# Kernel tuning notes

Measured on AMD Instinct MI355X. Metric: run time of the kernel, lower is better.

The kernel has to match this reference:

```python
import jax, jax.numpy as jnp
from jax import lax
import numpy as np

B, P, M1, M2, M3 = 128, 168, 2, 2, 2
M = M1 * M2 * M3
HIDC, HIDR, HIDS, CK, SKIP, HW = 50, 50, 5, 6, 24, 24
PT = (P - CK) // SKIP  # int((P-Ck)/skip) = 6
L = P - CK + 1         # 163


def gru(xs, w_ih, w_hh, b_ih, b_hh, hid):
    # xs: [T, N, in]; torch nn.GRU cell semantics, h0 = 0. Returns final h: [N, hid].
    def step(h, x):
        gi = x @ w_ih.T + b_ih
        gh = h @ w_hh.T + b_hh
        ir, iz, inn = jnp.split(gi, 3, axis=-1)
        hr, hz, hn = jnp.split(gh, 3, axis=-1)
        r = jax.nn.sigmoid(ir + hr)
        z = jax.nn.sigmoid(iz + hz)
        n = jnp.tanh(inn + r * hn)
        return (1.0 - z) * n + z * h, None
    h0 = jnp.zeros((xs.shape[1], hid), xs.dtype)
    h, _ = lax.scan(step, h0, xs)
    return h


def setup_inputs() -> dict:
    key = jax.random.key(0)
    ks = jax.random.split(key, 16)
    O = P * HIDC * CK  # 50400 conv output channels
    d = {
        'x': jax.random.normal(ks[0], (B, P, M1, M2, M3), jnp.float32),
        'conv_w': jax.random.normal(ks[1], (O, P, M1, M2, M3), jnp.float32) * 0.02,
        'conv_b': jax.random.normal(ks[2], (O,), jnp.float32) * 0.02,
        'g1_wih': jax.random.normal(ks[3], (3 * HIDR, HIDC), jnp.float32) * 0.1,
        'g1_whh': jax.random.normal(ks[4], (3 * HIDR, HIDR), jnp.float32) * 0.1,
        'g1_bih': jax.random.normal(ks[5], (3 * HIDR,), jnp.float32) * 0.1,
        'g1_bhh': jax.random.normal(ks[6], (3 * HIDR,), jnp.float32) * 0.1,
        'gs_wih': jax.random.normal(ks[7], (3 * HIDS, HIDC), jnp.float32) * 0.1,
        'gs_whh': jax.random.normal(ks[8], (3 * HIDS, HIDS), jnp.float32) * 0.1,
        'gs_bih': jax.random.normal(ks[9], (3 * HIDS,), jnp.float32) * 0.1,
        'gs_bhh': jax.random.normal(ks[10], (3 * HIDS,), jnp.float32) * 0.1,
        'l1_w': jax.random.normal(ks[11], (M, HIDR + SKIP * HIDS), jnp.float32) * 0.1,
        'l1_b': jax.random.normal(ks[12], (M,), jnp.float32) * 0.1,
        'hw_w': jax.random.normal(ks[13], (1, HW), jnp.float32) * 0.1,
        'hw_b': jax.random.normal(ks[14], (1,), jnp.float32) * 0.1,
    }
    return d


def reference(x, conv_w, conv_b, g1_wih, g1_whh, g1_bih, g1_bhh,
              gs_wih, gs_whh, gs_bih, gs_bhh, l1_w, l1_b, hw_w, hw_b):
    # Conv3d with kernel == full spatial extent is a dense matmul over (P*m1*m2*m3).
    xf = x.reshape(B, -1)                       # [B, P*M]
    wf = conv_w.reshape(conv_w.shape[0], -1)    # [O, P*M]
    c = jax.nn.relu(xf @ wf.T + conv_b)         # [B, O]
    c = c.reshape(B, HIDC, CK, P)
    # Diagonal strided sum (the torch triple loop): res1[b,c,t] = sum_k c[b,c,k,k+t]
    res1 = sum(c[:, :, k, k:k + L] for k in range(CK))  # [B, HIDC, L]
    # dropout: eval mode (identity)
    r = gru(jnp.transpose(res1, (2, 0, 1)), g1_wih, g1_whh, g1_bih, g1_bhh, HIDR)  # [B, HIDR]
    # skip GRU
    s = res1[:, :, -PT * SKIP:]                          # [B, HIDC, PT*SKIP]
    s = s.reshape(B, HIDC, PT, SKIP)
    s = jnp.transpose(s, (2, 0, 3, 1)).reshape(PT, B * SKIP, HIDC)
    hs = gru(s, gs_wih, gs_whh, gs_bih, gs_bhh, HIDS)    # [B*SKIP, HIDS]
    hs = hs.reshape(B, SKIP * HIDS)
    r = jnp.concatenate([r, hs], axis=1)                 # [B, HIDR + SKIP*HIDS]
    res = r @ l1_w.T + l1_b                              # [B, M]
    # highway (AR) component over the last HW timesteps
    z = x[:, -HW:].reshape(B, HW, M)                     # [B, HW, M]
    z = jnp.transpose(z, (0, 2, 1)).reshape(-1, HW)      # [B*M, HW]
    z = z @ hw_w.T + hw_b                                # [B*M, 1]
    res = res + z.reshape(B, M)
    res = jax.nn.sigmoid(res)
    return res.reshape(B, M1, M2, M3)
```

## Files before the change

### kernel.cpp

```cpp
#include <hip/hip_runtime.h>
#include <hip/hip_bf16.h>
#include <cstdint>


typedef __attribute__((ext_vector_type(8))) short short8;
typedef __attribute__((ext_vector_type(4))) float f32x4;

__device__ __forceinline__ unsigned short bf16rn(float f) {
    unsigned u = __float_as_uint(f);
    return (unsigned short)((u + 0x7FFFu + ((u >> 16) & 1u)) >> 16);
}
__device__ __forceinline__ unsigned pk2(float a, float b) {
    return ((unsigned)bf16rn(b) << 16) | (unsigned)bf16rn(a);
}
__device__ __forceinline__ uint4 pack8(float4 f0, float4 f1) {
    uint4 u;
    u.x = pk2(f0.x, f0.y); u.y = pk2(f0.z, f0.w);
    u.z = pk2(f1.x, f1.y); u.w = pk2(f1.z, f1.w);
    return u;
}
__device__ __forceinline__ float bf2f(unsigned short u) {
    return __uint_as_float((unsigned)u << 16);
}
__device__ __forceinline__ float sigmf(float x) { return 1.f / (1.f + __expf(-x)); }
__device__ __forceinline__ float tanhf_(float x) { return 1.f - 2.f / (__expf(2.f * x) + 1.f); }

__global__ __launch_bounds__(256, 2)
void k1_conv_gemm(const float* __restrict__ x, const float* __restrict__ w,
                  const float* __restrict__ bias, unsigned short* __restrict__ c) {
    __shared__ uint4 a_lds[8 * 129];
    __shared__ uint4 b_lds[8 * 113];
    const int tid  = threadIdx.x;
    const int n0   = blockIdx.x * 112;
    const int wave = tid >> 6, lane = tid & 63;
    const int quad = lane >> 4, m16 = lane & 15;

    f32x4 acc[2][7];
#pragma unroll
    for (int i = 0; i < 2; ++i)
#pragma unroll
        for (int j = 0; j < 7; ++j) acc[i][j] = (f32x4){0.f, 0.f, 0.f, 0.f};

    float4 pa[4][2];
    float4 pb[4][2];

    auto issue = [&](int kb) {
#pragma unroll
        for (int i = 0; i < 4; ++i) {
            int row = (tid >> 3) + 32 * i;
            const float* gp = x + row * 1344 + kb + (tid & 7) * 8;
            pa[i][0] = *reinterpret_cast<const float4*>(gp);
            pa[i][1] = *reinterpret_cast<const float4*>(gp + 4);
        }
#pragma unroll
        for (int i = 0; i < 4; ++i) {
            int idx = tid + 256 * i;
            if (idx < 896) {
                int row = idx >> 3;
                const float* gp = w + (size_t)(n0 + row) * 1344 + kb + (idx & 7) * 8;
                pb[i][0] = *reinterpret_cast<const float4*>(gp);
                pb[i][1] = *reinterpret_cast<const float4*>(gp + 4);
            }
        }
    };

    issue(0);
    for (int kb = 0; kb < 1344; kb += 64) {
#pragma unroll
        for (int i = 0; i < 4; ++i) {
            int idx = tid + 256 * i;
            int row = idx >> 3, ks = idx & 7;
            a_lds[ks * 129 + row] = pack8(pa[i][0], pa[i][1]);
        }
#pragma unroll
        for (int i = 0; i < 4; ++i) {
            int idx = tid + 256 * i;
            if (idx < 896) {
                int row = idx >> 3, ks = idx & 7;
                b_lds[ks * 113 + row] = pack8(pb[i][0], pb[i][1]);
            }
        }
        __syncthreads();
        if (kb + 64 < 1344) issue(kb + 64);
#pragma unroll
        for (int half = 0; half < 2; ++half) {
            const int kp = half * 4 + quad;
            short8 af[2], bfr[7];
#pragma unroll
            for (int rt = 0; rt < 2; ++rt)
                af[rt] = ((const short8*)a_lds)[kp * 129 + wave * 32 + rt * 16 + m16];
#pragma unroll
            for (int ct = 0; ct < 7; ++ct)
                bfr[ct] = ((const short8*)b_lds)[kp * 113 + ct * 16 + m16];
#pragma unroll
            for (int rt = 0; rt < 2; ++rt)
#pragma unroll
                for (int ct = 0; ct < 7; ++ct)
                    acc[rt][ct] = __builtin_amdgcn_mfma_f32_16x16x32_bf16(
                        af[rt], bfr[ct], acc[rt][ct], 0, 0, 0);
        }
        __syncthreads();
    }
#pragma unroll
    for (int ct = 0; ct < 7; ++ct) {
        int col = n0 + ct * 16 + m16;
        float bv = bias[col];
#pragma unroll
        for (int rt = 0; rt < 2; ++rt) {
#pragma unroll
            for (int r = 0; r < 4; ++r) {
                int grow = wave * 32 + rt * 16 + quad * 4 + r;
                float v = acc[rt][ct][r] + bv;
                v = fmaxf(v, 0.f);
                c[(size_t)grow * 50400 + col] = bf16rn(v);
            }
        }
    }
}

__global__ __launch_bounds__(256)
void k2_diag(const unsigned short* __restrict__ c, float* __restrict__ res1) {
    __shared__ float rloc[50 * 164];
    const int b = blockIdx.x;
    const unsigned short* cb = c + (size_t)b * 50400;
    for (int idx = threadIdx.x; idx < 8150; idx += 256) {
        int hc = idx / 163, t = idx - hc * 163;
        int base = hc * 1008 + t;
        float s = 0.f;
#pragma unroll
        for (int k = 0; k < 6; ++k) s += bf2f(cb[base + 169 * k]);
        rloc[hc * 164 + t] = s;
    }
    __syncthreads();
    for (int idx = threadIdx.x; idx < 8150; idx += 256) {
        int t = idx / 50, hc = idx - t * 50;
        res1[(size_t)(t * 128 + b) * 50 + hc] = rloc[hc * 164 + t];
    }
}

__global__ __launch_bounds__(256)
void k3_gi1(const float* __restrict__ res1, const float* __restrict__ wih,
            const float* __restrict__ bih, float* __restrict__ gi1) {
    __shared__ float wl[150 * 52];
    __shared__ float xl[64 * 52];
    const int row0 = blockIdx.x * 64;
    for (int idx = threadIdx.x; idx < 7500; idx += 256) {
        int r = idx / 50, j = idx - r * 50;
        wl[r * 52 + j] = wih[idx];
    }
    for (int idx = threadIdx.x; idx < 3200; idx += 256) {
        int r = idx / 50, j = idx - r * 50;
        xl[r * 52 + j] = res1[(size_t)row0 * 50 + idx];
    }
    __syncthreads();
    for (int e = threadIdx.x; e < 9600; e += 256) {
        int rr = e / 150, cc = e - rr * 150;
        float4 a0 = {0.f, 0.f, 0.f, 0.f};
        const float* xp = &xl[rr * 52];
        const float* wp = &wl[cc * 52];
#pragma unroll
        for (int j = 0; j < 48; j += 4) {
            float4 xv = *reinterpret_cast<const float4*>(xp + j);
            float4 wv = *reinterpret_cast<const float4*>(wp + j);
            a0.x += xv.x * wv.x; a0.y += xv.y * wv.y;
            a0.z += xv.z * wv.z; a0.w += xv.w * wv.w;
        }
        float acc = bih[cc] + xp[48] * wp[48] + xp[49] * wp[49]
                  + (a0.x + a0.y) + (a0.z + a0.w);
        gi1[(size_t)(row0 + rr) * 150 + cc] = acc;
    }
}

__global__ __launch_bounds__(256)
void k3_gi2(const float* __restrict__ res1, const float* __restrict__ wih,
            const float* __restrict__ bih, float* __restrict__ gi2) {
    __shared__ float wl[15 * 52];
    __shared__ float xl[64 * 52];
    const int row0 = blockIdx.x * 64;
    for (int idx = threadIdx.x; idx < 750; idx += 256) {
        int r = idx / 50, j = idx - r * 50;
        wl[r * 52 + j] = wih[idx];
    }
    for (int idx = threadIdx.x; idx < 3200; idx += 256) {
        int rr = idx / 50, j = idx - rr * 50;
        int r = row0 + rr;
        int pt = r / 3072, bsk = r - pt * 3072;
        int b = bsk / 24, sk = bsk - b * 24;
        int t = 19 + pt * 24 + sk;
        xl[rr * 52 + j] = res1[(size_t)(t * 128 + b) * 50 + j];
    }
    __syncthreads();
    for (int e = threadIdx.x; e < 960; e += 256) {
        int rr = e / 15, cc = e - rr * 15;
        float4 a0 = {0.f, 0.f, 0.f, 0.f};
        const float* xp = &xl[rr * 52];
        const float* wp = &wl[cc * 52];
#pragma unroll
        for (int j = 0; j < 48; j += 4) {
            float4 xv = *reinterpret_cast<const float4*>(xp + j);
            float4 wv = *reinterpret_cast<const float4*>(wp + j);
            a0.x += xv.x * wv.x; a0.y += xv.y * wv.y;
            a0.z += xv.z * wv.z; a0.w += xv.w * wv.w;
        }
        float acc = bih[cc] + xp[48] * wp[48] + xp[49] * wp[49]
                  + (a0.x + a0.y) + (a0.z + a0.w);
        gi2[(size_t)(row0 + rr) * 15 + cc] = acc;
    }
}

__global__ __launch_bounds__(64)
void k4_gru1(const float* __restrict__ gi1, const float* __restrict__ whh,
             const float* __restrict__ bhh, float* __restrict__ r1) {
    __shared__ float wl[7500];
    __shared__ __align__(16) float hl[2][64];
    const int b = blockIdx.x;
    const int l = threadIdx.x;
    for (int idx = l; idx < 7500; idx += 64) wl[idx] = whh[idx];
    hl[0][l] = 0.f;
    hl[1][l] = 0.f;
    __syncthreads();
    const int lc = (l < 50) ? l : 49;
    float wr[50], wz[50], wn[50];
#pragma unroll
    for (int j = 0; j < 50; ++j) {
        wr[j] = wl[lc * 50 + j];
        wz[j] = wl[(50 + lc) * 50 + j];
        wn[j] = wl[(100 + lc) * 50 + j];
    }
    const float bhr = bhh[lc], bhz = bhh[50 + lc], bhn = bhh[100 + lc];
    float hcur = 0.f;
    const float* gp = gi1 + (size_t)b * 150;
    float gir = gp[lc], giz = gp[50 + lc], gin = gp[100 + lc];
    int p = 0;
    for (int t = 0; t < 163; ++t) {
        float ngir = 0.f, ngiz = 0.f, ngin = 0.f;
        if (t < 162) {
            const float* gq = gp + 150 * 128;
            ngir = gq[lc]; ngiz = gq[50 + lc]; ngin = gq[100 + lc];
        }
        const float* hp = hl[p];
        float ar = bhr, az = bhz, an = bhn;
#pragma unroll
        for (int j4 = 0; j4 < 12; ++j4) {
            float4 hv = *reinterpret_cast<const float4*>(hp + 4 * j4);
            ar += wr[4 * j4 + 0] * hv.x + wr[4 * j4 + 1] * hv.y +
                  wr[4 * j4 + 2] * hv.z + wr[4 * j4 + 3] * hv.w;
            az += wz[4 * j4 + 0] * hv.x + wz[4 * j4 + 1] * hv.y +
                  wz[4 * j4 + 2] * hv.z + wz[4 * j4 + 3] * hv.w;
            an += wn[4 * j4 + 0] * hv.x + wn[4 * j4 + 1] * hv.y +
                  wn[4 * j4 + 2] * hv.z + wn[4 * j4 + 3] * hv.w;
        }
        {
            float h48 = hp[48], h49 = hp[49];
            ar += wr[48] * h48 + wr[49] * h49;
            az += wz[48] * h48 + wz[49] * h49;
            an += wn[48] * h48 + wn[49] * h49;
        }
        float rg = sigmf(gir + ar);
        float zg = sigmf(giz + az);
        float ng = tanhf_(gin + rg * an);
        float hn = (1.f - zg) * ng + zg * hcur;
        hl[1 - p][l] = hn;
        __syncthreads();
        p ^= 1;
        hcur = hn;
        gir = ngir; giz = ngiz; gin = ngin;
        gp += 150 * 128;
    }
    if (l < 50) r1[b * 50 + l] = hcur;
}

__global__ __launch_bounds__(256)
void k5_gru2(const float* __restrict__ gi2, const float* __restrict__ whh,
             const float* __restrict__ bhh, float* __restrict__ hs) {
    __shared__ float wl[75];
    __shared__ float bl[15];
    const int tid = threadIdx.x;
    if (tid < 75) wl[tid] = whh[tid];
    if (tid < 15) bl[tid] = bhh[tid];
    __syncthreads();
    const int bsk = blockIdx.x * 256 + tid;
    float h[5] = {0.f, 0.f, 0.f, 0.f, 0.f};
    for (int pt = 0; pt < 6; ++pt) {
        const float* gp = gi2 + (size_t)(pt * 3072 + bsk) * 15;
        float gi[15];
#pragma unroll
        for (int i = 0; i < 15; ++i) gi[i] = gp[i];
        float gh[15];
#pragma unroll
        for (int i = 0; i < 15; ++i) {
            float s = bl[i];
#pragma unroll
            for (int j = 0; j < 5; ++j) s += wl[i * 5 + j] * h[j];
            gh[i] = s;
        }
#pragma unroll
        for (int u = 0; u < 5; ++u) {
            float rg = sigmf(gi[u] + gh[u]);
            float zg = sigmf(gi[5 + u] + gh[5 + u]);
            float ng = tanhf_(gi[10 + u] + rg * gh[10 + u]);
            h[u] = (1.f - zg) * ng + zg * h[u];
        }
    }
#pragma unroll
    for (int u = 0; u < 5; ++u) hs[bsk * 5 + u] = h[u];
}

__global__ __launch_bounds__(256)
void k6_final(const float* __restrict__ r1, const float* __restrict__ hs,
              const float* __restrict__ l1w, const float* __restrict__ l1b,
              const float* __restrict__ x, const float* __restrict__ hww,
              const float* __restrict__ hwb, float* __restrict__ out) {
    const int tid = blockIdx.x * 256 + threadIdx.x;
    if (tid >= 1024) return;
    const int b = tid >> 3, m = tid & 7;
    float acc = l1b[m];
    const float* wrow = l1w + m * 170;
    const float* rb = r1 + b * 50;
#pragma unroll
    for (int j = 0; j < 50; ++j) acc += rb[j] * wrow[j];
    const float* hb = hs + b * 120;
#pragma unroll
    for (int j = 0; j < 120; ++j) acc += hb[j] * wrow[50 + j];
    float z = hwb[0];
    const float* xb = x + b * 1344 + 144 * 8 + m;
#pragma unroll
    for (int wi = 0; wi < 24; ++wi) z += xb[wi * 8] * hww[wi];
    out[tid] = 1.f / (1.f + __expf(-(acc + z)));
}

extern "C" void kernel_launch(void* const* d_in, const int* in_sizes, int n_in,
                              void* d_out, int out_size, void* d_ws, size_t ws_size,
                              hipStream_t stream) {
    const float* x      = (const float*)d_in[0];
    const float* conv_w = (const float*)d_in[1];
    const float* conv_b = (const float*)d_in[2];
    const float* g1_wih = (const float*)d_in[3];
    const float* g1_whh = (const float*)d_in[4];
    const float* g1_bih = (const float*)d_in[5];
    const float* g1_bhh = (const float*)d_in[6];
    const float* gs_wih = (const float*)d_in[7];
    const float* gs_whh = (const float*)d_in[8];
    const float* gs_bih = (const float*)d_in[9];
    const float* gs_bhh = (const float*)d_in[10];
    const float* l1_w   = (const float*)d_in[11];
    const float* l1_b   = (const float*)d_in[12];
    const float* hw_w   = (const float*)d_in[13];
    const float* hw_b   = (const float*)d_in[14];
    float* out = (float*)d_out;

    char* ws = (char*)d_ws;
    unsigned short* c   = (unsigned short*)(ws);
    float* res1         = (float*)(ws + 12902400);
    float* gi1          = (float*)(ws + 17075200);
    float* gi2          = (float*)(ws + 29593600);
    float* r1           = (float*)(ws + 30699520);
    float* hs           = (float*)(ws + 30725120);

    hipLaunchKernelGGL(k1_conv_gemm, dim3(450), dim3(256), 0, stream, x, conv_w, conv_b, c);
    hipLaunchKernelGGL(k2_diag,      dim3(128), dim3(256), 0, stream, c, res1);
    hipLaunchKernelGGL(k3_gi1,       dim3(326), dim3(256), 0, stream, res1, g1_wih, g1_bih, gi1);
    hipLaunchKernelGGL(k3_gi2,       dim3(288), dim3(256), 0, stream, res1, gs_wih, gs_bih, gi2);
    hipLaunchKernelGGL(k4_gru1,      dim3(128), dim3(64),  0, stream, gi1, g1_whh, g1_bhh, r1);
    hipLaunchKernelGGL(k5_gru2,      dim3(12),  dim3(256), 0, stream, gi2, gs_whh, gs_bhh, hs);
    hipLaunchKernelGGL(k6_final,     dim3(4),   dim3(256), 0, stream, r1, hs, l1_w, l1_b, x, hw_w, hw_b, out);
}
```

Baseline: 588.1 us.

## Fuse diagonal sum with GRU input projections into one per-batch kernel

Merges the diagonal strided-sum kernel with both GRU input-gate projection kernels, so each batch block keeps its res1 tile in shared memory and computes gi1 and gi2 directly. This removes the res1 global round trip and two kernel launches. In exchange the gi1 projection runs as a serial 163-step loop per thread over only 128 blocks, which lowers parallelism, and some threads in each block sit idle.

```diff
diff --git a/kernel.cpp b/kernel.cpp
--- a/kernel.cpp
+++ b/kernel.cpp
@@ -119,92 +119,79 @@
 }
 
 __global__ __launch_bounds__(256)
-void k2_diag(const unsigned short* __restrict__ c, float* __restrict__ res1) {
-    __shared__ float rloc[50 * 164];
+void k2f(const unsigned short* __restrict__ c,
+         const float* __restrict__ g1_wih, const float* __restrict__ g1_bih,
+         const float* __restrict__ gs_wih, const float* __restrict__ gs_bih,
+         float* __restrict__ gi1, float* __restrict__ gi2) {
+    __shared__ float xl[163 * 52];
+    __shared__ float wl1[150 * 52];
+    __shared__ float wl2[15 * 52];
+    __shared__ float bl2[15];
     const int b = blockIdx.x;
+    const int tid = threadIdx.x;
     const unsigned short* cb = c + (size_t)b * 50400;
-    for (int idx = threadIdx.x; idx < 8150; idx += 256) {
+
+    for (int i = tid; i < 7500; i += 256) {
+        int r = i / 50, j = i - r * 50;
+        wl1[r * 52 + j] = g1_wih[i];
+    }
+    for (int i = tid; i < 750; i += 256) {
+        int r = i / 50, j = i - r * 50;
+        wl2[r * 52 + j] = gs_wih[i];
+    }
+    if (tid < 15) bl2[tid] = gs_bih[tid];
+    for (int idx = tid; idx < 8150; idx += 256) {
         int hc = idx / 163, t = idx - hc * 163;
         int base = hc * 1008 + t;
         float s = 0.f;
 #pragma unroll
         for (int k = 0; k < 6; ++k) s += bf2f(cb[base + 169 * k]);
-        rloc[hc * 164 + t] = s;
+        xl[t * 52 + hc] = s;
     }
     __syncthreads();
-    for (int idx = threadIdx.x; idx < 8150; idx += 256) {
-        int t = idx / 50, hc = idx - t * 50;
-        res1[(size_t)(t * 128 + b) * 50 + hc] = rloc[hc * 164 + t];
-    }
-}
-
-__global__ __launch_bounds__(256)
-void k3_gi1(const float* __restrict__ res1, const float* __restrict__ wih,
-            const float* __restrict__ bih, float* __restrict__ gi1) {
-    __shared__ float wl[150 * 52];
-    __shared__ float xl[64 * 52];
-    const int row0 = blockIdx.x * 64;
-    for (int idx = threadIdx.x; idx < 7500; idx += 256) {
-        int r = idx / 50, j = idx - r * 50;
-        wl[r * 52 + j] = wih[idx];
-    }
-    for (int idx = threadIdx.x; idx < 3200; idx += 256) {
-        int r = idx / 50, j = idx - r * 50;
-        xl[r * 52 + j] = res1[(size_t)row0 * 50 + idx];
-    }
-    __syncthreads();
-    for (int e = threadIdx.x; e < 9600; e += 256) {
-        int rr = e / 150, cc = e - rr * 150;
-        float4 a0 = {0.f, 0.f, 0.f, 0.f};
-        const float* xp = &xl[rr * 52];
-        const float* wp = &wl[cc * 52];
-#pragma unroll
-        for (int j = 0; j < 48; j += 4) {
-            float4 xv = *reinterpret_cast<const float4*>(xp + j);
-            float4 wv = *reinterpret_cast<const float4*>(wp + j);
-            a0.x += xv.x * wv.x; a0.y += xv.y * wv.y;
-            a0.z += xv.z * wv.z; a0.w += xv.w * wv.w;
-        }
-        float acc = bih[cc] + xp[48] * wp[48] + xp[49] * wp[49]
-                  + (a0.x + a0.y) + (a0.z + a0.w);
-        gi1[(size_t)(row0 + rr) * 150 + cc] = acc;
-    }
-}
-
-__global__ __launch_bounds__(256)
-void k3_gi2(const float* __restrict__ res1, const float* __restrict__ wih,
-            const float* __restrict__ bih, float* __restrict__ gi2) {
-    __shared__ float wl[15 * 52];
-    __shared__ float xl[64 * 52];
-    const int row0 = blockIdx.x * 64;
-    for (int idx = threadIdx.x; idx < 750; idx += 256) {
-        int r = idx / 50, j = idx - r * 50;
-        wl[r * 52 + j] = wih[idx];
-    }
-    for (int idx = threadIdx.x; idx < 3200; idx += 256) {
-        int rr = idx / 50, j = idx - rr * 50;
-        int r = row0 + rr;
-        int pt = r / 3072, bsk = r - pt * 3072;
-        int b = bsk / 24, sk = bsk - b * 24;
-        int t = 19 + pt * 24 + sk;
-        xl[rr * 52 + j] = res1[(size_t)(t * 128 + b) * 50 + j];
-    }
-    __syncthreads();
-    for (int e = threadIdx.x; e < 960; e += 256) {
-        int rr = e / 15, cc = e - rr * 15;
-        float4 a0 = {0.f, 0.f, 0.f, 0.f};
-        const float* xp = &xl[rr * 52];
-        const float* wp = &wl[cc * 52];
-#pragma unroll
-        for (int j = 0; j < 48; j += 4) {
-            float4 xv = *reinterpret_cast<const float4*>(xp + j);
-            float4 wv = *reinterpret_cast<const float4*>(wp + j);
-            a0.x += xv.x * wv.x; a0.y += xv.y * wv.y;
-            a0.z += xv.z * wv.z; a0.w += xv.w * wv.w;
-        }
-        float acc = bih[cc] + xp[48] * wp[48] + xp[49] * wp[49]
-                  + (a0.x + a0.y) + (a0.z + a0.w);
-        gi2[(size_t)(row0 + rr) * 15 + cc] = acc;
+
+    if (tid < 150) {
+        const int cc = tid;
+        float wr[50];
+#pragma unroll
+        for (int j = 0; j < 48; j += 4)
+            *reinterpret_cast<float4*>(&wr[j]) =
+                *reinterpret_cast<const float4*>(&wl1[cc * 52 + j]);
+        wr[48] = wl1[cc * 52 + 48]; wr[49] = wl1[cc * 52 + 49];
+        const float bv = g1_bih[cc];
+        float* gout = gi1 + (size_t)b * 150 + cc;
+        for (int t = 0; t < 163; ++t) {
+            const float* xp = &xl[t * 52];
+            float4 a = {0.f, 0.f, 0.f, 0.f};
+#pragma unroll
+            for (int j = 0; j < 48; j += 4) {
+                float4 xv = *reinterpret_cast<const float4*>(xp + j);
+                a.x += xv.x * wr[j + 0]; a.y += xv.y * wr[j + 1];
+                a.z += xv.z * wr[j + 2]; a.w += xv.w * wr[j + 3];
+            }
+            float acc = bv + xp[48] * wr[48] + xp[49] * wr[49]
+                      + (a.x + a.y) + (a.z + a.w);
+            gout[(size_t)t * 128 * 150] = acc;
+        }
+    } else if (tid >= 192) {
+        for (int e = tid - 192; e < 2160; e += 64) {
+            int rr = e / 15, cc = e - rr * 15;
+            int pt = rr / 24, sk = rr - pt * 24;
+            int t = 19 + pt * 24 + sk;
+            const float* xp = &xl[t * 52];
+            const float* wp = &wl2[cc * 52];
+            float4 a = {0.f, 0.f, 0.f, 0.f};
+#pragma unroll
+            for (int j = 0; j < 48; j += 4) {
+                float4 xv = *reinterpret_cast<const float4*>(xp + j);
+                float4 wv = *reinterpret_cast<const float4*>(wp + j);
+                a.x += xv.x * wv.x; a.y += xv.y * wv.y;
+                a.z += xv.z * wv.z; a.w += xv.w * wv.w;
+            }
+            float acc = bl2[cc] + xp[48] * wp[48] + xp[49] * wp[49]
+                      + (a.x + a.y) + (a.z + a.w);
+            gi2[(size_t)(pt * 3072 + b * 24 + sk) * 15 + cc] = acc;
+        }
     }
 }
 
@@ -351,16 +338,14 @@
 
     char* ws = (char*)d_ws;
     unsigned short* c   = (unsigned short*)(ws);
-    float* res1         = (float*)(ws + 12902400);
-    float* gi1          = (float*)(ws + 17075200);
-    float* gi2          = (float*)(ws + 29593600);
-    float* r1           = (float*)(ws + 30699520);
-    float* hs           = (float*)(ws + 30725120);
+    float* gi1          = (float*)(ws + 12902400);
+    float* gi2          = (float*)(ws + 25420800);
+    float* r1           = (float*)(ws + 26526720);
+    float* hs           = (float*)(ws + 26552320);
 
     hipLaunchKernelGGL(k1_conv_gemm, dim3(450), dim3(256), 0, stream, x, conv_w, conv_b, c);
-    hipLaunchKernelGGL(k2_diag,      dim3(128), dim3(256), 0, stream, c, res1);
-    hipLaunchKernelGGL(k3_gi1,       dim3(326), dim3(256), 0, stream, res1, g1_wih, g1_bih, gi1);
-    hipLaunchKernelGGL(k3_gi2,       dim3(288), dim3(256), 0, stream, res1, gs_wih, gs_bih, gi2);
+    hipLaunchKernelGGL(k2f,          dim3(128), dim3(256), 0, stream, c, g1_wih, g1_bih,
+                       gs_wih, gs_bih, gi1, gi2);
     hipLaunchKernelGGL(k4_gru1,      dim3(128), dim3(64),  0, stream, gi1, g1_whh, g1_bhh, r1);
     hipLaunchKernelGGL(k5_gru2,      dim3(12),  dim3(256), 0, stream, gi2, gs_whh, gs_bhh, hs);
     hipLaunchKernelGGL(k6_final,     dim3(4),   dim3(256), 0, stream, r1, hs, l1_w, l1_b, x, hw_w, hw_b, out);
```

Result: no change. 592.8 us (+0.8%).
